# Kernel optimization log

Measured on AMD Instinct MI355X. Metric: run time of the kernel, lower is better.

Reference implementation:

```python
import math
import jax, jax.numpy as jnp
import numpy as np

B, T, D, H = 8, 2048, 1024, 32  # batch, positions, feature_dim, max_history (==T_hist)
DECAY_RATE = 0.95


def setup_inputs() -> dict:
    key = jax.random.key(0)
    ks = jax.random.split(key, 10)
    s = 1.0 / math.sqrt(D)
    inp = {
        "x": jax.random.normal(ks[0], (B, T, D), jnp.float32),
        "history": jax.random.normal(ks[1], (T, H, D), jnp.float32),  # [P=T, T_hist, D]
        "Wq": jax.random.normal(ks[2], (D, D), jnp.float32) * s,
        "bq": jnp.zeros((D,), jnp.float32),
        "Wk": jax.random.normal(ks[3], (D, D), jnp.float32) * s,
        "bk": jnp.zeros((D,), jnp.float32),
        "Wv": jax.random.normal(ks[4], (D, D), jnp.float32) * s,
        "bv": jnp.zeros((D,), jnp.float32),
        "Wo": jax.random.normal(ks[5], (D, D), jnp.float32) * s,
        "bo": jnp.zeros((D,), jnp.float32),
        "decay": jnp.asarray(DECAY_RATE ** np.arange(H), jnp.float32),
    }
    return inp


def reference(x, history, Wq, bq, Wk, bk, Wv, bv, Wo, bo, decay):
    # x: [B,T,D]; history: [T,T_hist,D]
    d = x.shape[-1]
    t_hist = history.shape[1]
    Q = x @ Wq.T + bq                       # [B,T,D]
    K = history @ Wk.T + bk                 # [T,T_hist,D]
    V = history @ Wv.T + bv                 # [T,T_hist,D]
    # per-position scores: Q[b,t,:] . K[t,h,:]
    scores = jnp.einsum('btd,thd->bth', Q, K) / jnp.sqrt(jnp.asarray(d, x.dtype))
    bias = jnp.log(decay[:t_hist][::-1] + 1e-10)  # [T_hist] (flipped, oldest gets smallest weight)
    attn = jax.nn.softmax(scores + bias, axis=-1)  # [B,T,T_hist]
    attended = jnp.einsum('bth,thd->btd', attn, V)  # [B,T,D]
    return (attended + x) @ Wo.T + bo
```

## Files before the change

### kernel.cpp

```cpp
#include <hip/hip_runtime.h>


#define BB 8
#define TT 2048
#define DD 1024
#define HH 32

typedef __attribute__((ext_vector_type(8))) short short8;
typedef __attribute__((ext_vector_type(4))) float f32x4;

__device__ __forceinline__ short f2b(float f) {
  unsigned u = __float_as_uint(f);
  unsigned r = u + 0x7fffu + ((u >> 16) & 1u);
  return (short)(r >> 16);
}

__device__ __forceinline__ void gload_lds16(const void* g, void* l) {
  __builtin_amdgcn_global_load_lds(
      (const __attribute__((address_space(1))) void*)g,
      (__attribute__((address_space(3))) void*)l, 16, 0, 0);
}

__global__ __launch_bounds__(256) void k_prep(
    const float* __restrict__ x, const float* __restrict__ Wq,
    const float* __restrict__ bq, const float* __restrict__ Wk,
    const float* __restrict__ Wv, const float* __restrict__ bv,
    const float* __restrict__ Wo, const float* __restrict__ bo,
    short* __restrict__ WqT, short* __restrict__ WkT, short* __restrict__ WvT,
    short* __restrict__ CC, short* __restrict__ WB, float* __restrict__ u3,
    float* __restrict__ bfin) {
  const int b = blockIdx.x;
  const int tid = threadIdx.x;
  if (b < 3072) {
    __shared__ float tile[32][33];
    const int z = b >> 10, rem = b & 1023;
    const float* src = z == 0 ? Wq : (z == 1 ? Wk : Wv);
    short* dst = z == 0 ? WqT : (z == 1 ? WkT : WvT);
    const int bx = (rem & 31) * 32, by = (rem >> 5) * 32;
    const int tx = tid & 31, ty = tid >> 5;
#pragma unroll
    for (int k = 0; k < 4; k++)
      tile[ty + 8 * k][tx] = src[(size_t)(by + ty + 8 * k) * DD + bx + tx];
    __syncthreads();
#pragma unroll
    for (int k = 0; k < 4; k++)
      dst[(size_t)(bx + ty + 8 * k) * DD + by + tx] = f2b(tile[tx][ty + 8 * k]);
  } else if (b < 11776) {
    const bool isx = b < 11264;
    const float* src = isx ? x : Wo;
    short* dst = isx ? CC : WB;
    size_t i = (((size_t)(b - (isx ? 3072 : 11264))) * 256 + tid) * 8;
    float4 a = *(const float4*)(src + i);
    float4 c = *(const float4*)(src + i + 4);
    short8 o;
    o[0] = f2b(a.x); o[1] = f2b(a.y); o[2] = f2b(a.z); o[3] = f2b(a.w);
    o[4] = f2b(c.x); o[5] = f2b(c.y); o[6] = f2b(c.z); o[7] = f2b(c.w);
    size_t r = i >> 10, cc = i & 1023;
    *(short8*)(dst + r * 2048 + 1024 + cc) = o;
  } else if (b < 11780) {
    const int d = (b - 11776) * 256 + tid;
    float a0 = 0, a1 = 0, a2 = 0, a3 = 0;
    for (int j = 0; j < DD; j += 4) {
      a0 = fmaf(Wk[(size_t)(j + 0) * DD + d], bq[j + 0], a0);
      a1 = fmaf(Wk[(size_t)(j + 1) * DD + d], bq[j + 1], a1);
      a2 = fmaf(Wk[(size_t)(j + 2) * DD + d], bq[j + 2], a2);
      a3 = fmaf(Wk[(size_t)(j + 3) * DD + d], bq[j + 3], a3);
    }
    u3[d] = (a0 + a1) + (a2 + a3);
  } else {
    const int j = b - 11780;
    float acc = 0.f;
    for (int d = tid; d < DD; d += 256) acc = fmaf(Wo[(size_t)j * DD + d], bv[d], acc);
#pragma unroll
    for (int off = 32; off >= 1; off >>= 1) acc += __shfl_down(acc, off);
    __shared__ float p[4];
    if ((tid & 63) == 0) p[tid >> 6] = acc;
    __syncthreads();
    if (tid == 0) bfin[j] = p[0] + p[1] + p[2] + p[3] + bo[j];
  }
}

__global__ __launch_bounds__(256) void k_gemm64x2(const short* __restrict__ WkT,
                                                  const short* __restrict__ WqT,
                                                  short* __restrict__ A2,
                                                  const short* __restrict__ WoB,
                                                  const short* __restrict__ WvT,
                                                  short* __restrict__ WB) {
  __shared__ short At[64 * 32];
  __shared__ short Bt[64 * 32];
  const short* A; const short* B; short* C; int lda, ldb, ldc;
  if (blockIdx.z == 0) {
    A = WkT; lda = 1024; B = WqT; ldb = 1024; C = A2; ldc = 1024;
  } else {
    A = WoB; lda = 2048; B = WvT; ldb = 1024; C = WB; ldc = 2048;
  }
  const int tid = threadIdx.x;
  const int w = tid >> 6, l = tid & 63;
  const int wm = w >> 1, wn = w & 1;
  const int lrow = l & 15, lk = l >> 4;
  const size_t m0 = (size_t)blockIdx.x * 64;
  const size_t n0 = (size_t)blockIdx.y * 64;

  f32x4 acc[2][2];
#pragma unroll
  for (int i = 0; i < 2; i++)
#pragma unroll
    for (int j = 0; j < 2; j++) acc[i][j] = (f32x4){0.f, 0.f, 0.f, 0.f};

  const unsigned ubase = (unsigned)((tid & ~63) * 16);
  const int r0 = tid >> 2, kc = tid & 3;

  for (int k0 = 0; k0 < 1024; k0 += 32) {
    __syncthreads();
    gload_lds16(A + (m0 + r0) * lda + k0 + kc * 8, (char*)At + ubase);
    gload_lds16(B + (n0 + r0) * ldb + k0 + kc * 8, (char*)Bt + ubase);
    __syncthreads();
    short8 af[2], bfv[2];
    const int aoff = (wm * 32 + lrow) * 32 + lk * 8;
    const int boff = (wn * 32 + lrow) * 32 + lk * 8;
#pragma unroll
    for (int mi = 0; mi < 2; mi++) af[mi] = *(const short8*)(At + aoff + mi * 512);
#pragma unroll
    for (int ni = 0; ni < 2; ni++) bfv[ni] = *(const short8*)(Bt + boff + ni * 512);
#pragma unroll
    for (int mi = 0; mi < 2; mi++)
#pragma unroll
      for (int ni = 0; ni < 2; ni++)
        acc[mi][ni] = __builtin_amdgcn_mfma_f32_16x16x32_bf16(af[mi], bfv[ni],
                                                              acc[mi][ni], 0, 0, 0);
  }

#pragma unroll
  for (int ni = 0; ni < 2; ni++) {
    const size_t col = n0 + wn * 32 + ni * 16 + lrow;
#pragma unroll
    for (int mi = 0; mi < 2; mi++) {
#pragma unroll
      for (int q = 0; q < 4; q++) {
        const size_t row = m0 + wm * 32 + mi * 16 + lk * 4 + q;
        C[row * ldc + col] = f2b(acc[mi][ni][q]);
      }
    }
  }
}

template <bool OUT_BF16>
__global__ __launch_bounds__(256) void k_gemm128(const short* __restrict__ A, int lda,
                                                 const short* __restrict__ B, int ldb,
                                                 void* __restrict__ Cv, int ldc, int K,
                                                 const float* __restrict__ bias,
                                                 int nblocks) {
  extern __shared__ char lds[];
  char* ldsA = lds;
  char* ldsB = lds + 49152;
  const int tid = threadIdx.x;
  const int w = tid >> 6;
  const int l = tid & 63;
  const int wm = w >> 1, wn = w & 1;
  const int lrow = l & 15, lk = l >> 4;

  const int nwg = gridDim.x;
  const int cpx = nwg >> 3;
  const int lin = blockIdx.x;
  const int wg = (lin & 7) * cpx + (lin >> 3);
  const int mb = wg / nblocks;
  const int nb = wg % nblocks;
  const size_t m0 = (size_t)mb * 128;
  const size_t n0 = (size_t)nb * 128;

  const int r = tid >> 3;
  const int kk0 = (((tid & 7) * 16) ^ ((r & 1) << 6)) >> 1;
  const short* pA0 = A + (m0 + r) * lda + kk0;
  const short* pA1 = A + (m0 + 32 + r) * lda + kk0;
  const short* pA2 = A + (m0 + 64 + r) * lda + kk0;
  const short* pA3 = A + (m0 + 96 + r) * lda + kk0;
  const short* pB0 = B + (n0 + r) * ldb + kk0;
  const short* pB1 = B + (n0 + 32 + r) * ldb + kk0;
  const short* pB2 = B + (n0 + 64 + r) * ldb + kk0;
  const short* pB3 = B + (n0 + 96 + r) * ldb + kk0;
  const unsigned wb16 = (unsigned)((tid & ~63) * 16);

  f32x4 acc[4][4];
#pragma unroll
  for (int i = 0; i < 4; i++)
#pragma unroll
    for (int j = 0; j < 4; j++) acc[i][j] = (f32x4){0.f, 0.f, 0.f, 0.f};

  const int NT = K >> 6;

#define STAGE_A(bufsel, koff)                                     \
  do {                                                            \
    char* ab_ = ldsA + (bufsel) * 16384;                          \
    gload_lds16(pA0 + (koff), ab_ + wb16);                        \
    gload_lds16(pA1 + (koff), ab_ + 4096 + wb16);                 \
    gload_lds16(pA2 + (koff), ab_ + 8192 + wb16);                 \
    gload_lds16(pA3 + (koff), ab_ + 12288 + wb16);                \
  } while (0)
#define STAGE_B(bufsel, koff)                                     \
  do {                                                            \
    char* bb_ = ldsB + (bufsel) * 16384;                          \
    gload_lds16(pB0 + (koff), bb_ + wb16);                        \
    gload_lds16(pB1 + (koff), bb_ + 4096 + wb16);                 \
    gload_lds16(pB2 + (koff), bb_ + 8192 + wb16);                 \
    gload_lds16(pB3 + (koff), bb_ + 12288 + wb16);                \
  } while (0)

  STAGE_B(0, 0);
  STAGE_A(0, 0);
  if (NT > 1) {
    STAGE_A(1, 64);
    asm volatile("s_waitcnt vmcnt(4)" ::: "memory");
  } else {
    asm volatile("s_waitcnt vmcnt(0)" ::: "memory");
  }
  __builtin_amdgcn_s_barrier();
  __builtin_amdgcn_sched_barrier(0);

  const int aswz = (lrow & 1) << 6;

  for (int kt = 0; kt < NT; ++kt) {
    const char* Ab = ldsA + (kt % 3) * 16384;
    const char* Bb = ldsB + (kt & 1) * 16384;

    short8 bfr[4][2];
#pragma unroll
    for (int ni = 0; ni < 4; ni++)
#pragma unroll
      for (int ks = 0; ks < 2; ks++) {
        const int ph =
            (((wn * 64 + ni * 16 + lrow) * 128 + ks * 64 + lk * 16)) ^ aswz;
        bfr[ni][ks] = *(const short8*)(Bb + ph);
      }
    if (kt + 1 < NT) STAGE_B((kt + 1) & 1, (size_t)(kt + 1) * 64);

    short8 af[4][2];
#pragma unroll
    for (int mi = 0; mi < 4; mi++)
#pragma unroll
      for (int ks = 0; ks < 2; ks++) {
        const int ph =
            (((wm * 64 + mi * 16 + lrow) * 128 + ks * 64 + lk * 16)) ^ aswz;
        af[mi][ks] = *(const short8*)(Ab + ph);
      }
    if (kt + 2 < NT) STAGE_A((kt + 2) % 3, (size_t)(kt + 2) * 64);

#pragma unroll
    for (int ks = 0; ks < 2; ks++)
#pragma unroll
      for (int mi = 0; mi < 4; mi++)
#pragma unroll
        for (int ni = 0; ni < 4; ni++)
          acc[mi][ni] = __builtin_amdgcn_mfma_f32_16x16x32_bf16(
              af[mi][ks], bfr[ni][ks], acc[mi][ni], 0, 0, 0);

    if (kt + 1 < NT) {
      if (kt + 2 < NT)
        asm volatile("s_waitcnt vmcnt(4)" ::: "memory");
      else
        asm volatile("s_waitcnt vmcnt(0)" ::: "memory");
      __builtin_amdgcn_s_barrier();
      __builtin_amdgcn_sched_barrier(0);
    }
  }
#undef STAGE_A
#undef STAGE_B

#pragma unroll
  for (int ni = 0; ni < 4; ni++) {
    const size_t col = n0 + wn * 64 + ni * 16 + lrow;
    const float bv_ = bias ? bias[col] : 0.f;
#pragma unroll
    for (int mi = 0; mi < 4; mi++) {
#pragma unroll
      for (int q = 0; q < 4; q++) {
        const size_t row = m0 + wm * 64 + mi * 16 + lk * 4 + q;
        const float v = acc[mi][ni][q] + bv_;
        if (OUT_BF16)
          ((short*)Cv)[row * ldc + col] = f2b(v);
        else
          ((float*)Cv)[row * ldc + col] = v;
      }
    }
  }
}

__global__ __launch_bounds__(512) void k_fused(const short* __restrict__ xA,
                                               const float* __restrict__ hist,
                                               const float* __restrict__ u3,
                                               const float* __restrict__ decay,
                                               short* __restrict__ CC) {
  extern __shared__ char smem[];
  short* histT = (short*)smem;
  float* spart = (float*)(smem + 65536);
  float* sfull = (float*)(smem + 65536 + 8192);
  short* attnb = (short*)(smem + 65536 + 8192 + 2048);

  const int t = blockIdx.x;
  const int tid = threadIdx.x;
  const int w = tid >> 6, l = tid & 63;
  const int lrow = l & 15, lk = l >> 4;

  f32x4 accs[2];
  accs[0] = (f32x4){0.f, 0.f, 0.f, 0.f};
  accs[1] = (f32x4){0.f, 0.f, 0.f, 0.f};

#pragma unroll
  for (int kk = 0; kk < 4; kk++) {
    const int ka = (w * 4 + kk) * 32 + lk * 8;
    short8 af;
    if (lrow < 8) {
      af = *(const short8*)(xA + ((size_t)lrow * TT + t) * DD + ka);
    } else if (lrow == 8) {
      const float* up = u3 + ka;
#pragma unroll
      for (int j = 0; j < 8; j++) af[j] = f2b(up[j]);
    } else {
#pragma unroll
      for (int j = 0; j < 8; j++) af[j] = 0;
    }
#pragma unroll
    for (int nt = 0; nt < 2; nt++) {
      const int h = lrow + nt * 16;
      const float* hp = hist + ((size_t)t * HH + h) * DD + ka;
      float4 h0 = *(const float4*)hp;
      float4 h1 = *(const float4*)(hp + 4);
      short8 bv_;
      bv_[0] = f2b(h0.x); bv_[1] = f2b(h0.y); bv_[2] = f2b(h0.z); bv_[3] = f2b(h0.w);
      bv_[4] = f2b(h1.x); bv_[5] = f2b(h1.y); bv_[6] = f2b(h1.z); bv_[7] = f2b(h1.w);
      accs[nt] = __builtin_amdgcn_mfma_f32_16x16x32_bf16(af, bv_, accs[nt], 0, 0, 0);
      const int hs = h >> 3, hl = h & 7;
#pragma unroll
      for (int j = 0; j < 8; j++) {
        const int d = ka + j;
        histT[(d << 5) + ((hs ^ ((d >> 1) & 3)) << 3) + hl] = bv_[j];
      }
    }
  }

  for (int half = 4; half >= 1; half >>= 1) {
    __syncthreads();
    if (w >= half && w < 2 * half) {
#pragma unroll
      for (int nt = 0; nt < 2; nt++)
#pragma unroll
        for (int q = 0; q < 4; q++)
          spart[(w - half) * 512 + (lk * 4 + q) * 32 + nt * 16 + lrow] = accs[nt][q];
    }
    __syncthreads();
    if (w < half) {
#pragma unroll
      for (int nt = 0; nt < 2; nt++)
#pragma unroll
        for (int q = 0; q < 4; q++)
          accs[nt][q] += spart[w * 512 + (lk * 4 + q) * 32 + nt * 16 + lrow];
    }
  }
  if (w == 0) {
#pragma unroll
    for (int nt = 0; nt < 2; nt++)
#pragma unroll
      for (int q = 0; q < 4; q++)
        sfull[(lk * 4 + q) * 32 + nt * 16 + lrow] = accs[nt][q];
  }
  __syncthreads();

  {
    const int bb = tid >> 5, h = tid & 31;
    float s = (sfull[bb * 32 + h] + sfull[8 * 32 + h]) * (1.0f / 32.0f) +
              logf(decay[31 - h] + 1e-10f);
    float m = s;
#pragma unroll
    for (int msk = 16; msk >= 1; msk >>= 1) m = fmaxf(m, __shfl_xor(m, msk));
    float p = expf(s - m);
    float den = p;
#pragma unroll
    for (int msk = 16; msk >= 1; msk >>= 1) den += __shfl_xor(den, msk);
    attnb[bb * 32 + h] = f2b(p / den);
  }
  __syncthreads();

  short8 paf = *(const short8*)(attnb + lrow * 32 + lk * 8);
  const f32x4 z4 = (f32x4){0.f, 0.f, 0.f, 0.f};
  float res[8][4];
#pragma unroll
  for (int i = 0; i < 8; i++) {
    const int d0 = (w * 8 + i) * 16;
    const int d = d0 + lrow;
    short8 hb = *(const short8*)(histT + (d << 5) + ((lk ^ ((d >> 1) & 3)) << 3));
    f32x4 o = __builtin_amdgcn_mfma_f32_16x16x32_bf16(paf, hb, z4, 0, 0, 0);
#pragma unroll
    for (int q = 0; q < 4; q++) res[i][q] = o[q];
  }
  __syncthreads();
  short* ah = histT;
  if (lk < 2) {
#pragma unroll
    for (int i = 0; i < 8; i++) {
      const int d = (w * 8 + i) * 16 + lrow;
#pragma unroll
      for (int q = 0; q < 4; q++) ah[(lk * 4 + q) * 1024 + d] = f2b(res[i][q]);
    }
  }
  __syncthreads();
  {
    const int b = tid >> 6, c0 = (tid & 63) * 16;
    short8 v0 = *(const short8*)(ah + b * 1024 + c0);
    short8 v1 = *(const short8*)(ah + b * 1024 + c0 + 8);
    short* dst = CC + ((size_t)b * TT + t) * 2048 + c0;
    *(short8*)dst = v0;
    *(short8*)(dst + 8) = v1;
  }
}

extern "C" void kernel_launch(void* const* d_in, const int* in_sizes, int n_in,
                              void* d_out, int out_size, void* d_ws, size_t ws_size,
                              hipStream_t stream) {
  (void)in_sizes; (void)n_in; (void)out_size; (void)ws_size;
  const float* x    = (const float*)d_in[0];
  const float* hist = (const float*)d_in[1];
  const float* Wq   = (const float*)d_in[2];
  const float* bq   = (const float*)d_in[3];
  const float* Wk   = (const float*)d_in[4];
  const float* Wv   = (const float*)d_in[6];
  const float* bv   = (const float*)d_in[7];
  const float* Wo   = (const float*)d_in[8];
  const float* bo   = (const float*)d_in[9];
  const float* dec  = (const float*)d_in[10];
  float* out = (float*)d_out;
  char* ws = (char*)d_ws;

  short* CC   = (short*)(ws + 0);
  short* xA   = (short*)(ws + 67108864);
  short* A2   = (short*)(ws + 100663296);
  short* WB   = (short*)(ws + 102760448);
  short* WqT  = (short*)(ws + 106954752);
  short* WkT  = (short*)(ws + 109051904);
  short* WvT  = (short*)(ws + 111149056);
  float* bfin = (float*)(ws + 113246208);
  float* u3   = (float*)(ws + 113250304);

  hipFuncSetAttribute((const void*)k_fused, hipFuncAttributeMaxDynamicSharedMemorySize,
                      76800);
  hipFuncSetAttribute((const void*)k_gemm128<true>,
                      hipFuncAttributeMaxDynamicSharedMemorySize, 81920);
  hipFuncSetAttribute((const void*)k_gemm128<false>,
                      hipFuncAttributeMaxDynamicSharedMemorySize, 81920);

  k_prep<<<12804, 256, 0, stream>>>(x, Wq, bq, Wk, Wv, bv, Wo, bo, WqT, WkT, WvT, CC,
                                    WB, u3, bfin);
  k_gemm64x2<<<dim3(16, 16, 2), 256, 0, stream>>>(WkT, WqT, A2, WB + 1024, WvT, WB);
  k_gemm128<true><<<1024, 256, 81920, stream>>>(CC + 1024, 2048, A2, 1024, xA, 1024,
                                                1024, nullptr, 8);
  k_fused<<<2048, 512, 76800, stream>>>(xA, hist, u3, dec, CC);
  k_gemm128<false><<<1024, 256, 81920, stream>>>(CC, 2048, WB, 2048, out, 1024, 2048,
                                                 bfin, 8);
}
```

Baseline: 277.6 us.

## Replace pipelined 128x128 GEMM with simple single-buffered K=32 LDS loop

The multi-stage software-pipelined GEMM (triple-buffered A, double-buffered B, K-step 64, swizzled LDS, manual waitcnt) is replaced by a straightforward kernel. The new kernel loads a 128x32 tile of A and of B into static shared memory each step, synchronizes twice, and runs MFMAs. It uses far less LDS (16KB instead of 80KB), which may raise occupancy, but it drops load/compute overlap and the LDS bank-conflict swizzle. Both GEMM launches use the new kernel.

Measured after the change: 315.8 us. +13.8%, slower.

```diff
diff --git a/kernel.cpp b/kernel.cpp
--- a/kernel.cpp
+++ b/kernel.cpp
@@ -145,17 +145,15 @@
 }
 
 template <bool OUT_BF16>
-__global__ __launch_bounds__(256) void k_gemm128(const short* __restrict__ A, int lda,
-                                                 const short* __restrict__ B, int ldb,
-                                                 void* __restrict__ Cv, int ldc, int K,
-                                                 const float* __restrict__ bias,
-                                                 int nblocks) {
-  extern __shared__ char lds[];
-  char* ldsA = lds;
-  char* ldsB = lds + 49152;
+__global__ __launch_bounds__(256) void k_gemm_m97(const short* __restrict__ A, int lda,
+                                                  const short* __restrict__ B, int ldb,
+                                                  void* __restrict__ Cv, int ldc, int K,
+                                                  const float* __restrict__ bias,
+                                                  int nblocks) {
+  __shared__ short At[128 * 32];
+  __shared__ short Bt[128 * 32];
   const int tid = threadIdx.x;
-  const int w = tid >> 6;
-  const int l = tid & 63;
+  const int w = tid >> 6, l = tid & 63;
   const int wm = w >> 1, wn = w & 1;
   const int lrow = l & 15, lk = l >> 4;
 
@@ -168,102 +166,36 @@
   const size_t m0 = (size_t)mb * 128;
   const size_t n0 = (size_t)nb * 128;
 
-  const int r = tid >> 3;
-  const int kk0 = (((tid & 7) * 16) ^ ((r & 1) << 6)) >> 1;
-  const short* pA0 = A + (m0 + r) * lda + kk0;
-  const short* pA1 = A + (m0 + 32 + r) * lda + kk0;
-  const short* pA2 = A + (m0 + 64 + r) * lda + kk0;
-  const short* pA3 = A + (m0 + 96 + r) * lda + kk0;
-  const short* pB0 = B + (n0 + r) * ldb + kk0;
-  const short* pB1 = B + (n0 + 32 + r) * ldb + kk0;
-  const short* pB2 = B + (n0 + 64 + r) * ldb + kk0;
-  const short* pB3 = B + (n0 + 96 + r) * ldb + kk0;
-  const unsigned wb16 = (unsigned)((tid & ~63) * 16);
-
   f32x4 acc[4][4];
 #pragma unroll
   for (int i = 0; i < 4; i++)
 #pragma unroll
     for (int j = 0; j < 4; j++) acc[i][j] = (f32x4){0.f, 0.f, 0.f, 0.f};
 
-  const int NT = K >> 6;
-
-#define STAGE_A(bufsel, koff)                                     \
-  do {                                                            \
-    char* ab_ = ldsA + (bufsel) * 16384;                          \
-    gload_lds16(pA0 + (koff), ab_ + wb16);                        \
-    gload_lds16(pA1 + (koff), ab_ + 4096 + wb16);                 \
-    gload_lds16(pA2 + (koff), ab_ + 8192 + wb16);                 \
-    gload_lds16(pA3 + (koff), ab_ + 12288 + wb16);                \
-  } while (0)
-#define STAGE_B(bufsel, koff)                                     \
-  do {                                                            \
-    char* bb_ = ldsB + (bufsel) * 16384;                          \
-    gload_lds16(pB0 + (koff), bb_ + wb16);                        \
-    gload_lds16(pB1 + (koff), bb_ + 4096 + wb16);                 \
-    gload_lds16(pB2 + (koff), bb_ + 8192 + wb16);                 \
-    gload_lds16(pB3 + (koff), bb_ + 12288 + wb16);                \
-  } while (0)
-
-  STAGE_B(0, 0);
-  STAGE_A(0, 0);
-  if (NT > 1) {
-    STAGE_A(1, 64);
-    asm volatile("s_waitcnt vmcnt(4)" ::: "memory");
-  } else {
-    asm volatile("s_waitcnt vmcnt(0)" ::: "memory");
-  }
-  __builtin_amdgcn_s_barrier();
-  __builtin_amdgcn_sched_barrier(0);
-
-  const int aswz = (lrow & 1) << 6;
-
-  for (int kt = 0; kt < NT; ++kt) {
-    const char* Ab = ldsA + (kt % 3) * 16384;
-    const char* Bb = ldsB + (kt & 1) * 16384;
-
-    short8 bfr[4][2];
-#pragma unroll
-    for (int ni = 0; ni < 4; ni++)
-#pragma unroll
-      for (int ks = 0; ks < 2; ks++) {
-        const int ph =
-            (((wn * 64 + ni * 16 + lrow) * 128 + ks * 64 + lk * 16)) ^ aswz;
-        bfr[ni][ks] = *(const short8*)(Bb + ph);
-      }
-    if (kt + 1 < NT) STAGE_B((kt + 1) & 1, (size_t)(kt + 1) * 64);
-
-    short8 af[4][2];
+  const unsigned ubase = (unsigned)((tid & ~63) * 16);
+  const int r0 = tid >> 2, kc = tid & 3;
+
+  for (int k0 = 0; k0 < K; k0 += 32) {
+    __syncthreads();
+    gload_lds16(A + (m0 + r0) * lda + k0 + kc * 8, (char*)At + ubase);
+    gload_lds16(A + (m0 + 64 + r0) * lda + k0 + kc * 8, (char*)At + 4096 + ubase);
+    gload_lds16(B + (n0 + r0) * ldb + k0 + kc * 8, (char*)Bt + ubase);
+    gload_lds16(B + (n0 + 64 + r0) * ldb + k0 + kc * 8, (char*)Bt + 4096 + ubase);
+    __syncthreads();
+    short8 af[4], bfv[4];
+    const int aoff = (wm * 64 + lrow) * 32 + lk * 8;
+    const int boff = (wn * 64 + lrow) * 32 + lk * 8;
+#pragma unroll
+    for (int mi = 0; mi < 4; mi++) af[mi] = *(const short8*)(At + aoff + mi * 512);
+#pragma unroll
+    for (int ni = 0; ni < 4; ni++) bfv[ni] = *(const short8*)(Bt + boff + ni * 512);
 #pragma unroll
     for (int mi = 0; mi < 4; mi++)
 #pragma unroll
-      for (int ks = 0; ks < 2; ks++) {
-        const int ph =
-            (((wm * 64 + mi * 16 + lrow) * 128 + ks * 64 + lk * 16)) ^ aswz;
-        af[mi][ks] = *(const short8*)(Ab + ph);
-      }
-    if (kt + 2 < NT) STAGE_A((kt + 2) % 3, (size_t)(kt + 2) * 64);
-
-#pragma unroll
-    for (int ks = 0; ks < 2; ks++)
-#pragma unroll
-      for (int mi = 0; mi < 4; mi++)
-#pragma unroll
-        for (int ni = 0; ni < 4; ni++)
-          acc[mi][ni] = __builtin_amdgcn_mfma_f32_16x16x32_bf16(
-              af[mi][ks], bfr[ni][ks], acc[mi][ni], 0, 0, 0);
-
-    if (kt + 1 < NT) {
-      if (kt + 2 < NT)
-        asm volatile("s_waitcnt vmcnt(4)" ::: "memory");
-      else
-        asm volatile("s_waitcnt vmcnt(0)" ::: "memory");
-      __builtin_amdgcn_s_barrier();
-      __builtin_amdgcn_sched_barrier(0);
-    }
-  }
-#undef STAGE_A
-#undef STAGE_B
+      for (int ni = 0; ni < 4; ni++)
+        acc[mi][ni] = __builtin_amdgcn_mfma_f32_16x16x32_bf16(af[mi], bfv[ni],
+                                                              acc[mi][ni], 0, 0, 0);
+  }
 
 #pragma unroll
   for (int ni = 0; ni < 4; ni++) {
@@ -441,17 +373,13 @@
 
   hipFuncSetAttribute((const void*)k_fused, hipFuncAttributeMaxDynamicSharedMemorySize,
                       76800);
-  hipFuncSetAttribute((const void*)k_gemm128<true>,
-                      hipFuncAttributeMaxDynamicSharedMemorySize, 81920);
-  hipFuncSetAttribute((const void*)k_gemm128<false>,
-                      hipFuncAttributeMaxDynamicSharedMemorySize, 81920);
 
   k_prep<<<12804, 256, 0, stream>>>(x, Wq, bq, Wk, Wv, bv, Wo, bo, WqT, WkT, WvT, CC,
                                     WB, u3, bfin);
   k_gemm64x2<<<dim3(16, 16, 2), 256, 0, stream>>>(WkT, WqT, A2, WB + 1024, WvT, WB);
-  k_gemm128<true><<<1024, 256, 81920, stream>>>(CC + 1024, 2048, A2, 1024, xA, 1024,
-                                                1024, nullptr, 8);
+  k_gemm_m97<true><<<1024, 256, 0, stream>>>(CC + 1024, 2048, A2, 1024, xA, 1024,
+                                             1024, nullptr, 8);
   k_fused<<<2048, 512, 76800, stream>>>(xA, hist, u3, dec, CC);
-  k_gemm128<false><<<1024, 256, 81920, stream>>>(CC, 2048, WB, 2048, out, 1024, 2048,
-                                                 bfin, 8);
-}
+  k_gemm_m97<false><<<1024, 256, 0, stream>>>(CC, 2048, WB, 2048, out, 1024, 2048,
+                                              bfin, 8);
+}
```
